# Kernel tuning notes

Hardware: AMD Instinct MI355X
Metric: run time of the kernel (lower is better)

Reference implementation:

```python
import jax, jax.numpy as jnp
import numpy as np
import math

B, S, D, H = 4, 2048, 1024, 16
DK = D // H

def setup_inputs() -> dict:
    key = jax.random.key(0)
    ks = jax.random.split(key, 12)
    scale = 1.0 / math.sqrt(D)
    inp = {
        "query": jax.random.normal(ks[0], (B, S, D), jnp.float32),
        "key_": jax.random.normal(ks[1], (B, S, D), jnp.float32),
        "value": jax.random.normal(ks[2], (B, S, D), jnp.float32),
        "mask": jnp.broadcast_to(jnp.tril(jnp.ones((S, S), jnp.int32)), (B, S, S)),
        "Wq": jax.random.normal(ks[3], (D, D), jnp.float32) * scale,
        "bq": jnp.zeros((D,), jnp.float32),
        "Wk": jax.random.normal(ks[4], (D, D), jnp.float32) * scale,
        "bk": jnp.zeros((D,), jnp.float32),
        "Wv": jax.random.normal(ks[5], (D, D), jnp.float32) * scale,
        "bv": jnp.zeros((D,), jnp.float32),
        "Wo": jax.random.normal(ks[6], (D, D), jnp.float32) * scale,
        "bo": jnp.zeros((D,), jnp.float32),
    }
    return inp

def reference(query, key_, value, mask, Wq, bq, Wk, bk, Wv, bv, Wo, bo):
    # Linear projections (torch Linear: x @ W^T + b), split into heads [B,H,S,DK]
    def proj(x, W, b):
        y = jnp.einsum('bsd,ed->bse', x, W) + b
        return y.reshape(B, S, H, DK).transpose(0, 2, 1, 3)
    Q = proj(query, Wq, bq)
    K = proj(key_, Wk, bk)
    V = proj(value, Wv, bv)
    # scaled dot-product attention with additive mask-fill
    scores = jnp.einsum('bhqd,bhkd->bhqk', Q, K) / math.sqrt(DK)
    scores = jnp.where(mask[:, None, :, :] == 0, jnp.float32(-1e9), scores)
    attn = jax.nn.softmax(scores, axis=-1)  # dropout p=0.0 (eval) -> identity
    ctx = jnp.einsum('bhqk,bhkd->bhqd', attn, V)
    ctx = ctx.transpose(0, 2, 1, 3).reshape(B, S, D)
    out = jnp.einsum('bsd,ed->bse', ctx, Wo) + bo
    return out
```

## Files before the change

### kernel.cpp

```cpp
#include <hip/hip_runtime.h>
#include <hip/hip_bf16.h>
#include <cstdint>
#include <cstddef>

static constexpr int kB = 4, kS = 2048, kD = 1024, kH = 16, kDK = 64;
static constexpr int kM = kB * kS;

typedef __attribute__((ext_vector_type(8))) __bf16 bf16x8;
typedef __attribute__((ext_vector_type(4))) float f32x4;

#define MFMA_BF16(a, b, c) __builtin_amdgcn_mfma_f32_16x16x32_bf16((a), (b), (c), 0, 0, 0)

#define GLDS16(gp, lp)                                                        \
  __builtin_amdgcn_global_load_lds(                                           \
      (__attribute__((address_space(1))) void*)(gp),                          \
      (__attribute__((address_space(3))) void*)(lp), 16, 0, 0)

__global__ __launch_bounds__(256) void cvt_f32_bf16(
    const float* __restrict__ src, __bf16* __restrict__ dst, int n8) {
  const int i = blockIdx.x * 256 + threadIdx.x;
  if (i >= n8) return;
  const float4 a = ((const float4*)src)[i * 2 + 0];
  const float4 b = ((const float4*)src)[i * 2 + 1];
  bf16x8 o;
  o[0] = (__bf16)a.x; o[1] = (__bf16)a.y; o[2] = (__bf16)a.z; o[3] = (__bf16)a.w;
  o[4] = (__bf16)b.x; o[5] = (__bf16)b.y; o[6] = (__bf16)b.z; o[7] = (__bf16)b.w;
  ((bf16x8*)dst)[i] = o;
}

template <int MODE, typename OutT>
__global__ __launch_bounds__(256) void gemm_bt(
    const __bf16* __restrict__ A, const __bf16* __restrict__ W,
    const float* __restrict__ bias, OutT* __restrict__ out) {
  __shared__ __align__(16) __bf16 As[128 * 32];
  __shared__ __align__(16) __bf16 Ws[128 * 32];
  const int tid = threadIdx.x;
  const int wave = tid >> 6, lane = tid & 63;
  const int col = lane & 15, quad = lane >> 4;
  const int m0 = (blockIdx.x & 63) * 128;
  const int n0 = (blockIdx.x >> 6) * 128;
  const int wr = (wave & 1) * 64, wc = (wave >> 1) * 64;

  f32x4 acc[4][4] = {};

  const int srow = tid >> 2;
  const int scol = (tid & 3) * 8;
  const __bf16* Ag = A + (size_t)(m0 + srow) * 1024 + scol;
  const __bf16* Wg = W + (size_t)(n0 + srow) * 1024 + scol;
  char* AsB = (char*)As + wave * 1024;
  char* WsB = (char*)Ws + wave * 1024;

  for (int k0 = 0; k0 < 1024; k0 += 32) {
    GLDS16(Ag + k0, AsB);
    GLDS16(Ag + k0 + (size_t)64 * 1024, AsB + 4096);
    GLDS16(Wg + k0, WsB);
    GLDS16(Wg + k0 + (size_t)64 * 1024, WsB + 4096);
    __syncthreads();
    bf16x8 af[4], wf[4];
#pragma unroll
    for (int t = 0; t < 4; ++t) {
      af[t] = *(const bf16x8*)&As[(wr + t * 16 + col) * 32 + quad * 8];
      wf[t] = *(const bf16x8*)&Ws[(wc + t * 16 + col) * 32 + quad * 8];
    }
#pragma unroll
    for (int rt = 0; rt < 4; ++rt)
#pragma unroll
      for (int ct = 0; ct < 4; ++ct)
        acc[rt][ct] = MFMA_BF16(af[rt], wf[ct], acc[rt][ct]);
    __syncthreads();
  }

#pragma unroll
  for (int ct = 0; ct < 4; ++ct) {
    const int n = n0 + wc + ct * 16 + col;
    const float bb = bias[n];
#pragma unroll
    for (int rt = 0; rt < 4; ++rt) {
#pragma unroll
      for (int r = 0; r < 4; ++r) {
        const int m = m0 + wr + rt * 16 + quad * 4 + r;
        const float v = acc[rt][ct][r] + bb;
        size_t idx;
        if (MODE == 0) {
          idx = (size_t)m * 1024 + n;
        } else {
          const int b = m >> 11, s = m & 2047;
          const int h = n >> 6, dk = n & 63;
          if (MODE == 1)
            idx = ((size_t)(b * 16 + h) * 2048 + s) * 64 + dk;
          else
            idx = ((size_t)(b * 16 + h) * 64 + dk) * 2048 + s;
        }
        out[idx] = (OutT)v;
      }
    }
  }
}

__global__ __launch_bounds__(256, 4) void flash_attn(
    const __bf16* __restrict__ Q, const __bf16* __restrict__ K,
    const __bf16* __restrict__ Vt, __bf16* __restrict__ ctx) {
  __shared__ __align__(16) __bf16 Ks[64 * 64];
  __shared__ __align__(16) __bf16 Vs[64 * 64];
  __shared__ __align__(16) __bf16 Pb[4][2][16 * 72];

  const int tid = threadIdx.x;
  const int wave = tid >> 6, lane = tid & 63;
  const int col = lane & 15, quad = lane >> 4;
  const int bh = blockIdx.x >> 4;
  const int pair = blockIdx.x & 15;
  const int b = bh >> 4, h = bh & 15;
  const int t_lo = pair, t_hi = 31 - pair;
  const int q0f[2] = {t_lo * 64 + wave * 16, t_hi * 64 + wave * 16};

  constexpr float SCL = 0.18033688011112042f;

  bf16x8 qf[2][2];
#pragma unroll
  for (int f = 0; f < 2; ++f) {
    const __bf16* Qp = Q + ((size_t)bh * kS + q0f[f] + col) * 64 + quad * 8;
    qf[f][0] = *(const bf16x8*)Qp;
    qf[f][1] = *(const bf16x8*)(Qp + 32);
  }

  f32x4 o[2][4] = {};
  f32x4 lacc[2] = {};
  bf16x8 ones;
#pragma unroll
  for (int i = 0; i < 8; ++i) ones[i] = (__bf16)1.0f;

  const __bf16* Kg = K + (size_t)bh * kS * 64;
  const __bf16* Vg = Vt + (size_t)bh * 64 * kS;

  const int row0 = tid >> 3, g0 = (tid & 7) ^ (row0 & 7);
  const int row1 = (256 + tid) >> 3, g1 = (tid & 7) ^ (row1 & 7);
  char* KsB = (char*)Ks + wave * 1024;
  char* VsB = (char*)Vs + wave * 1024;

  const int fgoff0 = ((quad) ^ (col & 7)) * 16;
  const int fgoff1 = ((quad + 4) ^ (col & 7)) * 16;
  const int maskbase = wave * 16 + quad * 4;

  __bf16* Pw0 = &Pb[wave][0][0];
  __bf16* Pw1 = &Pb[wave][1][0];
  const __bf16* Pr0 = Pw0 + col * 72 + quad * 8;
  const __bf16* Pr1 = Pw1 + col * 72 + quad * 8;

  auto body = [&](int c, bool lo, bool d0, bool d1) {
    const int k0 = c * 64;
    GLDS16(Kg + (size_t)(k0 + row0) * 64 + g0 * 8, KsB);
    GLDS16(Vg + (size_t)row0 * kS + k0 + g0 * 8, VsB);
    GLDS16(Kg + (size_t)(k0 + row1) * 64 + g1 * 8, KsB + 4096);
    GLDS16(Vg + (size_t)row1 * kS + k0 + g1 * 8, VsB + 4096);
    __syncthreads();

    f32x4 s[2][4];
#pragma unroll
    for (int kt = 0; kt < 4; ++kt) {
      const char* kp = (const char*)Ks + (kt * 16 + col) * 128;
      const bf16x8 kf0 = *(const bf16x8*)(kp + fgoff0);
      const bf16x8 kf1 = *(const bf16x8*)(kp + fgoff1);
      f32x4 z = {};
      s[1][kt] = MFMA_BF16(qf[1][1], kf1, MFMA_BF16(qf[1][0], kf0, z));
      if (lo) s[0][kt] = MFMA_BF16(qf[0][1], kf1, MFMA_BF16(qf[0][0], kf0, z));
    }
#pragma unroll
    for (int kt = 0; kt < 4; ++kt) {
#pragma unroll
      for (int r = 0; r < 4; ++r) {
        float pv1 = __builtin_amdgcn_exp2f(s[1][kt][r] * SCL);
        if (d1 && (kt * 16 + col > maskbase + r)) pv1 = 0.0f;
        Pw1[(quad * 4 + r) * 72 + kt * 16 + col] = (__bf16)pv1;
        if (lo) {
          float pv0 = __builtin_amdgcn_exp2f(s[0][kt][r] * SCL);
          if (d0 && (kt * 16 + col > maskbase + r)) pv0 = 0.0f;
          Pw0[(quad * 4 + r) * 72 + kt * 16 + col] = (__bf16)pv0;
        }
      }
    }
    __threadfence_block();
    const bf16x8 pf1a = *(const bf16x8*)Pr1;
    const bf16x8 pf1b = *(const bf16x8*)(Pr1 + 32);
    bf16x8 pf0a = {}, pf0b = {};
    if (lo) {
      pf0a = *(const bf16x8*)Pr0;
      pf0b = *(const bf16x8*)(Pr0 + 32);
    }
#pragma unroll
    for (int dt = 0; dt < 4; ++dt) {
      const char* vp = (const char*)Vs + (dt * 16 + col) * 128;
      const bf16x8 vf0 = *(const bf16x8*)(vp + fgoff0);
      const bf16x8 vf1 = *(const bf16x8*)(vp + fgoff1);
      o[1][dt] = MFMA_BF16(pf1b, vf1, MFMA_BF16(pf1a, vf0, o[1][dt]));
      if (lo) o[0][dt] = MFMA_BF16(pf0b, vf1, MFMA_BF16(pf0a, vf0, o[0][dt]));
    }
    lacc[1] = MFMA_BF16(pf1b, ones, MFMA_BF16(pf1a, ones, lacc[1]));
    if (lo) lacc[0] = MFMA_BF16(pf0b, ones, MFMA_BF16(pf0a, ones, lacc[0]));
    __syncthreads();
  };

  for (int c = 0; c <= t_lo; ++c) body(c, true, c == t_lo, false);
  for (int c = t_lo + 1; c <= t_hi; ++c) body(c, false, false, c == t_hi);

#pragma unroll
  for (int f = 0; f < 2; ++f) {
#pragma unroll
    for (int r = 0; r < 4; ++r) {
      const float inv = 1.0f / lacc[f][r];
      const int srow = q0f[f] + quad * 4 + r;
      __bf16* cp = ctx + ((size_t)b * kS + srow) * kD + h * 64 + col;
#pragma unroll
      for (int dt = 0; dt < 4; ++dt)
        cp[dt * 16] = (__bf16)(o[f][dt][r] * inv);
    }
  }
}

extern "C" void kernel_launch(void* const* d_in, const int* in_sizes, int n_in,
                              void* d_out, int out_size, void* d_ws, size_t ws_size,
                              hipStream_t stream) {
  const float* query = (const float*)d_in[0];
  const float* key_  = (const float*)d_in[1];
  const float* value = (const float*)d_in[2];
  const float* Wq = (const float*)d_in[4];
  const float* bq = (const float*)d_in[5];
  const float* Wk = (const float*)d_in[6];
  const float* bk = (const float*)d_in[7];
  const float* Wv = (const float*)d_in[8];
  const float* bv = (const float*)d_in[9];
  const float* Wo = (const float*)d_in[10];
  const float* bo = (const float*)d_in[11];

  const size_t elems = (size_t)kM * kD;
  const size_t welems = (size_t)kD * kD;
  __bf16* Qw = (__bf16*)d_ws;
  __bf16* Kw = Qw + elems;
  __bf16* Vw = Kw + elems;
  __bf16* Ab = Vw + elems;
  __bf16* Wb = Ab + elems;
  float* out = (float*)d_out;

  const int actg = (int)(elems / 8 / 256);
  const int wg   = (int)(welems / 8 / 256);

  cvt_f32_bf16<<<actg, 256, 0, stream>>>(query, Ab, (int)(elems / 8));
  cvt_f32_bf16<<<wg, 256, 0, stream>>>(Wq, Wb, (int)(welems / 8));
  gemm_bt<1, __bf16><<<512, 256, 0, stream>>>(Ab, Wb, bq, Qw);
  cvt_f32_bf16<<<actg, 256, 0, stream>>>(key_, Ab, (int)(elems / 8));
  cvt_f32_bf16<<<wg, 256, 0, stream>>>(Wk, Wb, (int)(welems / 8));
  gemm_bt<1, __bf16><<<512, 256, 0, stream>>>(Ab, Wb, bk, Kw);
  cvt_f32_bf16<<<actg, 256, 0, stream>>>(value, Ab, (int)(elems / 8));
  cvt_f32_bf16<<<wg, 256, 0, stream>>>(Wv, Wb, (int)(welems / 8));
  gemm_bt<2, __bf16><<<512, 256, 0, stream>>>(Ab, Wb, bv, Vw);
  flash_attn<<<kB * kH * 16, 256, 0, stream>>>(Qw, Kw, Vw, Ab);
  cvt_f32_bf16<<<wg, 256, 0, stream>>>(Wo, Wb, (int)(welems / 8));
  gemm_bt<0, float><<<512, 256, 0, stream>>>(Ab, Wb, bo, out);
}
```

Measured before the change: 373.2 us.

## Batch conversions and QKV GEMMs into single launches; widen K tile with XOR swizzle

Merges the three activation conversions and four weight conversions into two batched kernels, and runs the Q/K/V projections as one 1536-block GEMM launch. This cuts the number of launches and lets the three projections fill the GPU together. The GEMM core now loads a 64-wide K slice per iteration into an XOR-swizzled LDS layout, which halves the barrier count and avoids bank conflicts. The batched path needs a larger workspace and falls back to the old sequence when the workspace is too small. LDS per block doubles, which may reduce occupancy.

```diff
diff --git a/kernel.cpp b/kernel.cpp
--- a/kernel.cpp
+++ b/kernel.cpp
@@ -16,57 +16,93 @@
       (__attribute__((address_space(1))) void*)(gp),                          \
       (__attribute__((address_space(3))) void*)(lp), 16, 0, 0)
 
+__device__ __forceinline__ bf16x8 cvt8(const float* s, int i) {
+  const float4 a = ((const float4*)s)[i * 2 + 0];
+  const float4 b = ((const float4*)s)[i * 2 + 1];
+  bf16x8 o;
+  o[0] = (__bf16)a.x; o[1] = (__bf16)a.y; o[2] = (__bf16)a.z; o[3] = (__bf16)a.w;
+  o[4] = (__bf16)b.x; o[5] = (__bf16)b.y; o[6] = (__bf16)b.z; o[7] = (__bf16)b.w;
+  return o;
+}
+
 __global__ __launch_bounds__(256) void cvt_f32_bf16(
     const float* __restrict__ src, __bf16* __restrict__ dst, int n8) {
   const int i = blockIdx.x * 256 + threadIdx.x;
   if (i >= n8) return;
-  const float4 a = ((const float4*)src)[i * 2 + 0];
-  const float4 b = ((const float4*)src)[i * 2 + 1];
-  bf16x8 o;
-  o[0] = (__bf16)a.x; o[1] = (__bf16)a.y; o[2] = (__bf16)a.z; o[3] = (__bf16)a.w;
-  o[4] = (__bf16)b.x; o[5] = (__bf16)b.y; o[6] = (__bf16)b.z; o[7] = (__bf16)b.w;
-  ((bf16x8*)dst)[i] = o;
-}
-
-template <int MODE, typename OutT>
-__global__ __launch_bounds__(256) void gemm_bt(
+  ((bf16x8*)dst)[i] = cvt8(src, i);
+}
+
+__global__ __launch_bounds__(256) void cvt_act3(
+    const float* __restrict__ a, const float* __restrict__ b,
+    const float* __restrict__ c, __bf16* __restrict__ da,
+    __bf16* __restrict__ db, __bf16* __restrict__ dc) {
+  const int seg = blockIdx.x >> 12;
+  const int i = (blockIdx.x & 4095) * 256 + threadIdx.x;
+  const float* s = seg == 0 ? a : seg == 1 ? b : c;
+  __bf16* d = seg == 0 ? da : seg == 1 ? db : dc;
+  ((bf16x8*)d)[i] = cvt8(s, i);
+}
+
+__global__ __launch_bounds__(256) void cvt_w4(
+    const float* __restrict__ a, const float* __restrict__ b,
+    const float* __restrict__ c, const float* __restrict__ d,
+    __bf16* __restrict__ da, __bf16* __restrict__ db,
+    __bf16* __restrict__ dc, __bf16* __restrict__ dd) {
+  const int seg = blockIdx.x >> 9;
+  const int i = (blockIdx.x & 511) * 256 + threadIdx.x;
+  const float* s = seg == 0 ? a : seg == 1 ? b : seg == 2 ? c : d;
+  __bf16* o = seg == 0 ? da : seg == 1 ? db : seg == 2 ? dc : dd;
+  ((bf16x8*)o)[i] = cvt8(s, i);
+}
+
+template <typename OutT>
+__device__ __forceinline__ void gemm_core(
     const __bf16* __restrict__ A, const __bf16* __restrict__ W,
-    const float* __restrict__ bias, OutT* __restrict__ out) {
-  __shared__ __align__(16) __bf16 As[128 * 32];
-  __shared__ __align__(16) __bf16 Ws[128 * 32];
+    const float* __restrict__ bias, OutT* __restrict__ out, int mode, int bid,
+    __bf16* As, __bf16* Ws) {
   const int tid = threadIdx.x;
   const int wave = tid >> 6, lane = tid & 63;
   const int col = lane & 15, quad = lane >> 4;
-  const int m0 = (blockIdx.x & 63) * 128;
-  const int n0 = (blockIdx.x >> 6) * 128;
+  const int m0 = (bid & 63) * 128;
+  const int n0 = (bid >> 6) * 128;
   const int wr = (wave & 1) * 64, wc = (wave >> 1) * 64;
 
   f32x4 acc[4][4] = {};
 
-  const int srow = tid >> 2;
-  const int scol = (tid & 3) * 8;
-  const __bf16* Ag = A + (size_t)(m0 + srow) * 1024 + scol;
-  const __bf16* Wg = W + (size_t)(n0 + srow) * 1024 + scol;
-  char* AsB = (char*)As + wave * 1024;
-  char* WsB = (char*)Ws + wave * 1024;
-
-  for (int k0 = 0; k0 < 1024; k0 += 32) {
-    GLDS16(Ag + k0, AsB);
-    GLDS16(Ag + k0 + (size_t)64 * 1024, AsB + 4096);
-    GLDS16(Wg + k0, WsB);
-    GLDS16(Wg + k0 + (size_t)64 * 1024, WsB + 4096);
+  int srow[4], sgo[4];
+#pragma unroll
+  for (int i = 0; i < 4; ++i) {
+    const int s = i * 256 + tid;
+    srow[i] = s >> 3;
+    sgo[i] = (((s & 7) ^ ((s >> 3) & 7))) * 8;
+  }
+  const int g0 = ((quad) ^ (col & 7)) * 16;
+  const int g1 = ((quad + 4) ^ (col & 7)) * 16;
+
+  for (int k0 = 0; k0 < 1024; k0 += 64) {
+#pragma unroll
+    for (int i = 0; i < 4; ++i) {
+      GLDS16(A + (size_t)(m0 + srow[i]) * 1024 + k0 + sgo[i],
+             (char*)As + i * 4096 + wave * 1024);
+      GLDS16(W + (size_t)(n0 + srow[i]) * 1024 + k0 + sgo[i],
+             (char*)Ws + i * 4096 + wave * 1024);
+    }
     __syncthreads();
-    bf16x8 af[4], wf[4];
-#pragma unroll
-    for (int t = 0; t < 4; ++t) {
-      af[t] = *(const bf16x8*)&As[(wr + t * 16 + col) * 32 + quad * 8];
-      wf[t] = *(const bf16x8*)&Ws[(wc + t * 16 + col) * 32 + quad * 8];
-    }
-#pragma unroll
-    for (int rt = 0; rt < 4; ++rt)
-#pragma unroll
-      for (int ct = 0; ct < 4; ++ct)
-        acc[rt][ct] = MFMA_BF16(af[rt], wf[ct], acc[rt][ct]);
+#pragma unroll
+    for (int h = 0; h < 2; ++h) {
+      const int go = h ? g1 : g0;
+      bf16x8 af[4], wf[4];
+#pragma unroll
+      for (int t = 0; t < 4; ++t) {
+        af[t] = *(const bf16x8*)((const char*)As + (wr + t * 16 + col) * 128 + go);
+        wf[t] = *(const bf16x8*)((const char*)Ws + (wc + t * 16 + col) * 128 + go);
+      }
+#pragma unroll
+      for (int rt = 0; rt < 4; ++rt)
+#pragma unroll
+        for (int ct = 0; ct < 4; ++ct)
+          acc[rt][ct] = MFMA_BF16(af[rt], wf[ct], acc[rt][ct]);
+    }
     __syncthreads();
   }
 
@@ -81,12 +117,12 @@
         const int m = m0 + wr + rt * 16 + quad * 4 + r;
         const float v = acc[rt][ct][r] + bb;
         size_t idx;
-        if (MODE == 0) {
+        if (mode == 0) {
           idx = (size_t)m * 1024 + n;
         } else {
           const int b = m >> 11, s = m & 2047;
           const int h = n >> 6, dk = n & 63;
-          if (MODE == 1)
+          if (mode == 1)
             idx = ((size_t)(b * 16 + h) * 2048 + s) * 64 + dk;
           else
             idx = ((size_t)(b * 16 + h) * 64 + dk) * 2048 + s;
@@ -95,6 +131,33 @@
       }
     }
   }
+}
+
+template <int MODE, typename OutT>
+__global__ __launch_bounds__(256) void gemm_one(
+    const __bf16* __restrict__ A, const __bf16* __restrict__ W,
+    const float* __restrict__ bias, OutT* __restrict__ out) {
+  __shared__ __align__(16) __bf16 As[128 * 64];
+  __shared__ __align__(16) __bf16 Ws[128 * 64];
+  gemm_core<OutT>(A, W, bias, out, MODE, blockIdx.x, As, Ws);
+}
+
+__global__ __launch_bounds__(256) void gemm_qkv(
+    const __bf16* __restrict__ Aq, const __bf16* __restrict__ Ak,
+    const __bf16* __restrict__ Av, const __bf16* __restrict__ Wqb,
+    const __bf16* __restrict__ Wkb, const __bf16* __restrict__ Wvb,
+    const float* __restrict__ bq, const float* __restrict__ bk,
+    const float* __restrict__ bv, __bf16* __restrict__ Qw,
+    __bf16* __restrict__ Kw, __bf16* __restrict__ Vw) {
+  __shared__ __align__(16) __bf16 As[128 * 64];
+  __shared__ __align__(16) __bf16 Ws[128 * 64];
+  const int seg = blockIdx.x >> 9;
+  const int bid = blockIdx.x & 511;
+  const __bf16* A = seg == 0 ? Aq : seg == 1 ? Ak : Av;
+  const __bf16* W = seg == 0 ? Wqb : seg == 1 ? Wkb : Wvb;
+  const float* bias = seg == 0 ? bq : seg == 1 ? bk : bv;
+  __bf16* out = seg == 0 ? Qw : seg == 1 ? Kw : Vw;
+  gemm_core<__bf16>(A, W, bias, out, seg == 2 ? 2 : 1, bid, As, Ws);
 }
 
 __global__ __launch_bounds__(256, 4) void flash_attn(
@@ -231,28 +294,50 @@
   const float* Wo = (const float*)d_in[10];
   const float* bo = (const float*)d_in[11];
 
-  const size_t elems = (size_t)kM * kD;
-  const size_t welems = (size_t)kD * kD;
-  __bf16* Qw = (__bf16*)d_ws;
-  __bf16* Kw = Qw + elems;
-  __bf16* Vw = Kw + elems;
-  __bf16* Ab = Vw + elems;
-  __bf16* Wb = Ab + elems;
+  const size_t e = (size_t)kM * kD;
+  const size_t w = (size_t)kD * kD;
   float* out = (float*)d_out;
 
-  const int actg = (int)(elems / 8 / 256);
-  const int wg   = (int)(welems / 8 / 256);
-
-  cvt_f32_bf16<<<actg, 256, 0, stream>>>(query, Ab, (int)(elems / 8));
-  cvt_f32_bf16<<<wg, 256, 0, stream>>>(Wq, Wb, (int)(welems / 8));
-  gemm_bt<1, __bf16><<<512, 256, 0, stream>>>(Ab, Wb, bq, Qw);
-  cvt_f32_bf16<<<actg, 256, 0, stream>>>(key_, Ab, (int)(elems / 8));
-  cvt_f32_bf16<<<wg, 256, 0, stream>>>(Wk, Wb, (int)(welems / 8));
-  gemm_bt<1, __bf16><<<512, 256, 0, stream>>>(Ab, Wb, bk, Kw);
-  cvt_f32_bf16<<<actg, 256, 0, stream>>>(value, Ab, (int)(elems / 8));
-  cvt_f32_bf16<<<wg, 256, 0, stream>>>(Wv, Wb, (int)(welems / 8));
-  gemm_bt<2, __bf16><<<512, 256, 0, stream>>>(Ab, Wb, bv, Vw);
-  flash_attn<<<kB * kH * 16, 256, 0, stream>>>(Qw, Kw, Vw, Ab);
-  cvt_f32_bf16<<<wg, 256, 0, stream>>>(Wo, Wb, (int)(welems / 8));
-  gemm_bt<0, float><<<512, 256, 0, stream>>>(Ab, Wb, bo, out);
-}
+  const size_t REQ = (6 * e + 4 * w) * sizeof(__bf16);
+
+  if (ws_size >= REQ) {
+    __bf16* Qw  = (__bf16*)d_ws;
+    __bf16* Kw  = Qw + e;
+    __bf16* Vw  = Kw + e;
+    __bf16* Aq  = Vw + e;
+    __bf16* Ak  = Aq + e;
+    __bf16* Av  = Ak + e;
+    __bf16* Wqb = Av + e;
+    __bf16* Wkb = Wqb + w;
+    __bf16* Wvb = Wkb + w;
+    __bf16* Wob = Wvb + w;
+
+    cvt_act3<<<3 * 4096, 256, 0, stream>>>(query, key_, value, Aq, Ak, Av);
+    cvt_w4<<<4 * 512, 256, 0, stream>>>(Wq, Wk, Wv, Wo, Wqb, Wkb, Wvb, Wob);
+    gemm_qkv<<<1536, 256, 0, stream>>>(Aq, Ak, Av, Wqb, Wkb, Wvb, bq, bk, bv,
+                                       Qw, Kw, Vw);
+    flash_attn<<<kB * kH * 16, 256, 0, stream>>>(Qw, Kw, Vw, Aq);
+    gemm_one<0, float><<<512, 256, 0, stream>>>(Aq, Wob, bo, out);
+  } else {
+    __bf16* Qw = (__bf16*)d_ws;
+    __bf16* Kw = Qw + e;
+    __bf16* Vw = Kw + e;
+    __bf16* Ab = Vw + e;
+    __bf16* Wb = Ab + e;
+
+    const int actg = (int)(e / 8 / 256);
+    const int wg = (int)(w / 8 / 256);
+    cvt_f32_bf16<<<actg, 256, 0, stream>>>(query, Ab, (int)(e / 8));
+    cvt_f32_bf16<<<wg, 256, 0, stream>>>(Wq, Wb, (int)(w / 8));
+    gemm_one<1, __bf16><<<512, 256, 0, stream>>>(Ab, Wb, bq, Qw);
+    cvt_f32_bf16<<<actg, 256, 0, stream>>>(key_, Ab, (int)(e / 8));
+    cvt_f32_bf16<<<wg, 256, 0, stream>>>(Wk, Wb, (int)(w / 8));
+    gemm_one<1, __bf16><<<512, 256, 0, stream>>>(Ab, Wb, bk, Kw);
+    cvt_f32_bf16<<<actg, 256, 0, stream>>>(value, Ab, (int)(e / 8));
+    cvt_f32_bf16<<<wg, 256, 0, stream>>>(Wv, Wb, (int)(w / 8));
+    gemm_one<2, __bf16><<<512, 256, 0, stream>>>(Ab, Wb, bv, Vw);
+    flash_attn<<<kB * kH * 16, 256, 0, stream>>>(Qw, Kw, Vw, Ab);
+    cvt_f32_bf16<<<wg, 256, 0, stream>>>(Wo, Wb, (int)(w / 8));
+    gemm_one<0, float><<<512, 256, 0, stream>>>(Ab, Wb, bo, out);
+  }
+}
```

After: 357.0 us. -4.3%, faster.
